# Kernel tuning notes

Measured on AMD Instinct MI355X. Metric: run time of the kernel, lower is better.

Reference implementation:

```python
import jax, jax.numpy as jnp
import numpy as np

TAU = 2.0          # LIF membrane time constant
SG_ALPHA = 4.0     # sigmoid surrogate-gradient sharpness (spikingjelly default)
TIM_ALPHA = 0.6
EPS_BN = 1e-5
NUM_HEADS = 8

@jax.custom_vjp
def spike(u):
    return (u >= 0.0).astype(u.dtype)

def _spike_fwd(u):
    return spike(u), u

def _spike_bwd(u, g):
    s = jax.nn.sigmoid(SG_ALPHA * u)
    return (g * SG_ALPHA * s * (1.0 - s),)

spike.defvjp(_spike_fwd, _spike_bwd)

def lif(x, vth):
    # Multi-step LIF over leading time axis; v_reset=0, detach_reset=True.
    def step(v, xt):
        v = v + (xt - v) / TAU
        s = spike(v - vth)
        v = v * (1.0 - jax.lax.stop_gradient(s))
        return v, s
    _, out = jax.lax.scan(step, jnp.zeros_like(x[0]), x)
    return out

def bn_c(x, p):
    # x: [T,B,C,H,W]; p: [4,C] rows = (gamma, beta, mean, var); inference BN
    g, b, m, v = p
    inv = g * jax.lax.rsqrt(v + EPS_BN)
    return inv[:, None, None] * (x - m[:, None, None]) + b[:, None, None]

def bn_last(x, p):
    # channel on last axis
    g, b, m, v = p
    return g * jax.lax.rsqrt(v + EPS_BN) * (x - m) + b

def tim(q, w, b):
    # q: [T,B,C,H,W]. Conv1d (kernel 5, pad 2) over flattened spatial dim,
    # recurrent temporal interaction, then output LIF (vth=0.5).
    T, B, C, H, W = q.shape
    x = q.reshape(T, B, C, H * W)
    dn = ('NCH', 'OIH', 'NCH')
    outs = [x[0]]
    x_tim = x[0]
    for i in range(1, T):  # T is small and fixed
        c = jax.lax.conv_general_dilated(x_tim, w, (1,), [(2, 2)], dimension_numbers=dn)
        c = c + b[None, :, None]
        s = lif(c[None], 0.3)[0]
        x_tim = s * TIM_ALPHA + x[i] * (1.0 - TIM_ALPHA)
        outs.append(x_tim)
    out = lif(jnp.stack(outs), 0.5)
    return out.reshape(T, B, C, H, W)

def dssa_forward(x, wq, wk, wv, k_bn, v_bn, dst_w, dst_bn, proj_w, proj_b, proj_bn, tim_w, tim_b):
    T, B, C, H, W = x.shape
    NH = NUM_HEADS
    hd = C // NH
    N = H * W
    identity = x

    xs = lif(x, 1.0)  # shortcut LIF
    # 1x1 convs are channel matmuls
    q = lif(jnp.einsum('tbchw,dc->tbdhw', xs, wq), 0.05)   # note: no BN on q path (as in source)
    q = tim(q, tim_w, tim_b)
    k = lif(bn_c(jnp.einsum('tbchw,dc->tbdhw', xs, wk), k_bn), 1.0)
    v = lif(bn_c(jnp.einsum('tbchw,dc->tbdhw', xs, wv), v_bn), 1.0)

    def to_heads(z):  # [T,B,C,H,W] -> [T,B,NH,N,hd]
        return z.reshape(T, B, NH, hd, N).transpose(0, 1, 2, 4, 3)
    q, k, v = to_heads(q), to_heads(k), to_heads(v)

    # dst_conv with sr_ratio=1 is a 1x1 conv on head_dim channels; shared dst_bn
    k_t = bn_last(jnp.einsum('tbhnd,ed->tbhne', k, dst_w), dst_bn)
    v_t = bn_last(jnp.einsum('tbhnd,ed->tbhne', v, dst_w), dst_bn)

    attn = jnp.einsum('tbhnd,tbhmd->tbhnm', q, k_t)
    c1 = jnp.minimum(1.0 / jnp.sqrt(q.mean() * hd + 1e-6), 10.0)  # firing-rate scale
    attn_map = lif(attn * c1, 0.5)  # spiking attention map

    out = jnp.einsum('tbhnm,tbhmd->tbhnd', attn_map, v_t)
    out = out.transpose(0, 1, 2, 4, 3).reshape(T, B, C, H, W)
    out = out + identity
    out = jnp.einsum('tbchw,dc->tbdhw', out, proj_w) + proj_b[None, None, :, None, None]
    out = lif(bn_c(out, proj_bn), 1.0)
    return out, v


def setup_inputs() -> dict:
    key = jax.random.key(0)
    ks = jax.random.split(key, 12)
    T, B, C, H, W = 4, 16, 384, 16, 16
    hd = C // NUM_HEADS

    def bn_params(k, c):
        return jnp.stack([
            jnp.ones((c,), jnp.float32),                              # gamma
            jnp.zeros((c,), jnp.float32),                             # beta
            0.1 * jax.random.normal(k, (c,), jnp.float32),            # running mean
            0.5 + jax.random.uniform(jax.random.fold_in(k, 1), (c,), jnp.float32),  # running var
        ])

    s = (2.0 / C) ** 0.5
    return {
        'x': jax.random.normal(ks[0], (T, B, C, H, W), jnp.float32),
        'wq': s * jax.random.normal(ks[1], (C, C), jnp.float32),
        'wk': s * jax.random.normal(ks[2], (C, C), jnp.float32),
        'wv': s * jax.random.normal(ks[3], (C, C), jnp.float32),
        'k_bn': bn_params(ks[4], C),
        'v_bn': bn_params(ks[5], C),
        'dst_w': (2.0 / hd) ** 0.5 * jax.random.normal(ks[6], (hd, hd), jnp.float32),
        'dst_bn': bn_params(ks[7], hd),
        'proj_w': s * jax.random.normal(ks[8], (C, C), jnp.float32),
        'proj_b': jnp.zeros((C,), jnp.float32),
        'proj_bn': bn_params(ks[9], C),
        'tim_w': (2.0 / (C * 5)) ** 0.5 * jax.random.normal(ks[10], (C, C, 5), jnp.float32),
        'tim_b': jnp.zeros((C,), jnp.float32),
    }


def reference(x, wq, wk, wv, k_bn, v_bn, dst_w, dst_bn, proj_w, proj_b, proj_bn, tim_w, tim_b):
    return dssa_forward(x, wq, wk, wv, k_bn, v_bn, dst_w, dst_bn, proj_w, proj_b, proj_bn, tim_w, tim_b)
```

## Files before the change

kernel.cpp:

```cpp
#include <hip/hip_runtime.h>
#include <math.h>

#define TT 4
#define BB 16
#define CC 384
#define NS 256
#define NHD 8
#define HDD 48
#define PLANE 98304
#define TSTR  1572864
#define TOT   6291456
#define CCSQ  147456
#define PB    99840
#define PPL   1597440

#define OFF_XS   0L
#define OFF_Q    (1L*TOT)
#define OFF_K    (2L*TOT)
#define OFF_V    (3L*TOT)
#define OFF_OUTS (4L*TOT)
#define OFF_KTS  (11L*TOT/2)
#define OFF_VT   (7L*TOT)
#define OFF_CNT  (8L*TOT)

#define NPART 6144

typedef __attribute__((ext_vector_type(8))) short short8;
typedef __attribute__((ext_vector_type(4))) float f32x4;

__device__ __forceinline__ ushort f2bf(float x) {
    union { float f; unsigned u; } c; c.f = x;
    unsigned r = c.u + 0x7FFFu + ((c.u >> 16) & 1u);
    return (ushort)(r >> 16);
}
__device__ __forceinline__ float bf2f(ushort h) {
    union { unsigned u; float f; } c; c.u = ((unsigned)h) << 16;
    return c.f;
}

__global__ __launch_bounds__(256) void k_lif_x_t(const float* __restrict__ x,
                                                 ushort* __restrict__ xs)
{
    int b = blockIdx.z, c0 = blockIdx.y*64, n0 = blockIdx.x*64;
    __shared__ ushort T[64][72];
    int tid = threadIdx.x;
    int row = tid >> 2;
    int col4 = tid & 3;

    float v[16];
    #pragma unroll
    for (int i = 0; i < 16; i++) v[i] = 0.f;

    for (int t = 0; t < TT; t++) {
        __syncthreads();
        #pragma unroll
        for (int rep = 0; rep < 4; rep++) {
            int j = col4 + rep*4;
            float4 xv = *(const float4*)&x[(long)t*TSTR + (long)b*PLANE + (long)(c0+row)*NS + n0 + j*4];
            #pragma unroll
            for (int jj = 0; jj < 4; jj++) {
                int idx = rep*4 + jj;
                float xt = ((const float*)&xv)[jj];
                float vv = v[idx];
                vv += (xt - vv)*0.5f;
                float s = (vv - 1.0f) >= 0.f ? 1.f : 0.f;
                T[j*4+jj][row] = (s != 0.f) ? (ushort)0x3F80 : (ushort)0;
                v[idx] = vv*(1.f - s);
            }
        }
        __syncthreads();
        #pragma unroll
        for (int rep = 0; rep < 2; rep++) {
            int nrow = tid >> 2;
            int cq = (tid & 3) + rep*4;
            *(uint4*)&xs[(long)t*TSTR + (long)b*PLANE + (long)(n0+nrow)*CC + c0 + cq*8]
                = *(uint4*)&T[nrow][cq*8];
        }
    }
}

__global__ __launch_bounds__(256) void k_zero_pads(unsigned* __restrict__ qspT_u32)
{
    int i = blockIdx.x*256 + threadIdx.x;
    int plane = i / 768, rem = i % 768;
    int r = rem / 192, cu = rem % 192;
    int row = (r < 2) ? r : (256 + r);
    qspT_u32[(long)plane*(PB/2) + row*192 + cu] = 0;
}

__global__ __launch_bounds__(256) void k_wsplit(
    const float* __restrict__ wq, const float* __restrict__ wk, const float* __restrict__ wv,
    ushort* __restrict__ wsp)
{
    int i = blockIdx.x*256 + threadIdx.x;
    int which = i / CCSQ, r = i % CCSQ;
    const float* W = (which==0) ? wq : (which==1 ? wk : wv);
    float v = W[r];
    ushort hi = f2bf(v);  float r1 = v - bf2f(hi);
    ushort md = f2bf(r1); float r2 = r1 - bf2f(md);
    ushort lo = f2bf(r2);
    long b = (long)which*3*CCSQ;
    wsp[b + r] = hi; wsp[b + CCSQ + r] = md; wsp[b + 2L*CCSQ + r] = lo;
}

__global__ __launch_bounds__(256) void k_wsplit_tim(const float* __restrict__ tw,
                                                    ushort* __restrict__ timw)
{
    int i = blockIdx.x*256 + threadIdx.x;
    const float* src = tw + (long)i*5;
    #pragma unroll
    for (int tap = 0; tap < 5; tap++) {
        float v = src[tap];
        ushort hi = f2bf(v);  float r1 = v - bf2f(hi);
        ushort md = f2bf(r1); float r2 = r1 - bf2f(md);
        ushort lo = f2bf(r2);
        timw[(long)(0*5 + tap)*CCSQ + i] = hi;
        timw[(long)(1*5 + tap)*CCSQ + i] = md;
        timw[(long)(2*5 + tap)*CCSQ + i] = lo;
    }
}

__global__ __launch_bounds__(512) void k_gemm_qkv_mfma(
    const ushort* __restrict__ wsp,
    const float* __restrict__ kbn, const float* __restrict__ vbn,
    const ushort* __restrict__ xs,
    float* __restrict__ qo, float* __restrict__ ko, float* __restrict__ vo)
{
    int which = blockIdx.y >> 6;
    int tb    = blockIdx.y & 63;
    const ushort* X = xs + (long)tb*PLANE;
    const ushort* Wb = wsp + (long)which*3*CCSQ;
    int d0 = blockIdx.x*64;

    __shared__ ushort Ws[3][64][40];
    __shared__ ushort Xs[256][40];

    int tid = threadIdx.x, lane = tid & 63, w = tid >> 6;
    int q4 = lane >> 4, l16 = lane & 15;
    int dstrip = w & 3, nh = w >> 2;

    f32x4 acc[8];
    #pragma unroll
    for (int nt = 0; nt < 8; nt++) acc[nt] = (f32x4){0.f,0.f,0.f,0.f};

    for (int k0 = 0; k0 < CC; k0 += 32) {
        __syncthreads();
        for (int idx = tid; idx < 1792; idx += 512) {
            if (idx < 768) {
                int pl = idx >> 8, rem = idx & 255;
                int d = rem >> 2, c8 = rem & 3;
                *(uint4*)&Ws[pl][d][c8*8] =
                    *(const uint4*)(Wb + (long)pl*CCSQ + (long)(d0+d)*CC + k0 + c8*8);
            } else {
                int j = idx - 768;
                int n = j >> 2, c8 = j & 3;
                *(uint4*)&Xs[n][c8*8] = *(const uint4*)(X + (long)n*CC + k0 + c8*8);
            }
        }
        __syncthreads();

        short8 wh = *(short8*)&Ws[0][dstrip*16 + l16][q4*8];
        short8 wm = *(short8*)&Ws[1][dstrip*16 + l16][q4*8];
        short8 wl = *(short8*)&Ws[2][dstrip*16 + l16][q4*8];
        #pragma unroll
        for (int nt = 0; nt < 8; nt++) {
            short8 xr = *(short8*)&Xs[nh*128 + nt*16 + l16][q4*8];
            acc[nt] = __builtin_amdgcn_mfma_f32_16x16x32_bf16(xr, wh, acc[nt], 0, 0, 0);
            acc[nt] = __builtin_amdgcn_mfma_f32_16x16x32_bf16(xr, wm, acc[nt], 0, 0, 0);
            acc[nt] = __builtin_amdgcn_mfma_f32_16x16x32_bf16(xr, wl, acc[nt], 0, 0, 0);
        }
    }

    float* Y = ((which==0) ? qo : (which==1 ? ko : vo)) + (long)tb*PLANE;
    int d = d0 + dstrip*16 + l16;
    float inv = 1.f, mu = 0.f, be = 0.f;
    if (which != 0) {
        const float* bn = (which==1) ? kbn : vbn;
        float g = bn[d]; be = bn[CC+d]; mu = bn[2*CC+d]; float va = bn[3*CC+d];
        inv = g / sqrtf(va + 1e-5f);
    }
    #pragma unroll
    for (int nt = 0; nt < 8; nt++) {
        #pragma unroll
        for (int r = 0; r < 4; r++) {
            int n = nh*128 + nt*16 + q4*4 + r;
            float v = acc[nt][r];
            if (which != 0) v = inv*(v - mu) + be;
            Y[(long)n*CC + d] = v;
        }
    }
}

__global__ __launch_bounds__(256) void k_lif_qkv(
    const float* __restrict__ qb, const float* __restrict__ kb, const float* __restrict__ vb,
    ushort* __restrict__ qspT, ushort* __restrict__ ksp, ushort* __restrict__ vsp,
    float* __restrict__ vout)
{
    int which = blockIdx.y;
    int i = blockIdx.x*256 + threadIdx.x;
    const float* rbuf = (which==0) ? qb : (which==1 ? kb : vb);
    float vth  = (which==0) ? 0.05f : 1.0f;
    int b = i / PLANE;
    long qofs = (long)i + b*1536 + 768;
    int c=0, n2=0, h=0, dd=0;
    if (which == 2) {
        c = i % CC; n2 = (i / CC) % NS;
        h = c / HDD; dd = c % HDD;
    }
    float v = 0.f;
    #pragma unroll
    for (int t = 0; t < TT; t++) {
        float xt = rbuf[t*TSTR + i];
        v += (xt - v)*0.5f;
        float s = (v - vth) >= 0.f ? 1.f : 0.f;
        ushort sb = (s != 0.f) ? (ushort)0x3F80 : (ushort)0;
        if (which == 0)      qspT[(long)t*PPL + qofs] = sb;
        else if (which == 1) ksp[(long)t*TSTR + i] = sb;
        else {
            vsp[(long)t*TSTR + i] = sb;
            vout[(((long)(t*BB+b)*NHD + h)*NS + n2)*HDD + dd] = s;
        }
        v *= (1.f - s);
    }
}

__global__ __launch_bounds__(512) void k_tim_conv_mfma(
    const ushort* __restrict__ timw, const float* __restrict__ bias,
    const ushort* __restrict__ qT,
    const ushort* __restrict__ sTp,
    int hass,
    ushort* __restrict__ sTo)
{
    int b = blockIdx.z, d0 = blockIdx.y*64, n0 = blockIdx.x*64;
    const ushort* qp = qT  + (long)b*PB;
    const ushort* sp = sTp + (long)b*PB;

    __shared__ ushort Xs[2][68][40];

    int tid = threadIdx.x, lane = tid & 63, w = tid >> 6;
    int q4 = lane >> 4, l16 = lane & 15;
    int dstrip = w >> 1, nh = w & 1;

    const ushort* wb = timw + (long)(d0 + dstrip*16 + l16)*CC;

    f32x4 accQ[2], accS[2];
    #pragma unroll
    for (int nt = 0; nt < 2; nt++) {
        accQ[nt] = (f32x4){0.f,0.f,0.f,0.f};
        accS[nt] = (f32x4){0.f,0.f,0.f,0.f};
    }

    for (int c0 = 0; c0 < CC; c0 += 32) {
        __syncthreads();
        int tot = hass ? 544 : 272;
        for (int idx = tid; idx < tot; idx += 512) {
            int tsel = (idx >= 272) ? 1 : 0;
            int rr = idx - tsel*272;
            int r = rr >> 2, c8 = rr & 3;
            const ushort* src = (tsel ? sp : qp) + (long)(n0 + r)*CC + c0 + c8*8;
            *(uint4*)&Xs[tsel][r][c8*8] = *(const uint4*)src;
        }
        __syncthreads();

        #pragma unroll
        for (int tap = 0; tap < 5; tap++) {
            short8 w0 = *(const short8*)(wb + (long)(0*5 + tap)*CCSQ + c0 + q4*8);
            short8 w1 = *(const short8*)(wb + (long)(1*5 + tap)*CCSQ + c0 + q4*8);
            short8 w2 = *(const short8*)(wb + (long)(2*5 + tap)*CCSQ + c0 + q4*8);
            #pragma unroll
            for (int nt = 0; nt < 2; nt++) {
                int row = nh*32 + nt*16 + l16 + tap;
                short8 aq = *(short8*)&Xs[0][row][q4*8];
                accQ[nt] = __builtin_amdgcn_mfma_f32_16x16x32_bf16(aq, w0, accQ[nt], 0, 0, 0);
                accQ[nt] = __builtin_amdgcn_mfma_f32_16x16x32_bf16(aq, w1, accQ[nt], 0, 0, 0);
                accQ[nt] = __builtin_amdgcn_mfma_f32_16x16x32_bf16(aq, w2, accQ[nt], 0, 0, 0);
                if (hass) {
                    short8 as = *(short8*)&Xs[1][row][q4*8];
                    accS[nt] = __builtin_amdgcn_mfma_f32_16x16x32_bf16(as, w0, accS[nt], 0, 0, 0);
                    accS[nt] = __builtin_amdgcn_mfma_f32_16x16x32_bf16(as, w1, accS[nt], 0, 0, 0);
                    accS[nt] = __builtin_amdgcn_mfma_f32_16x16x32_bf16(as, w2, accS[nt], 0, 0, 0);
                }
            }
        }
    }

    ushort* so = sTo + (long)b*PB;
    int d = d0 + dstrip*16 + l16;
    float bv = bias[d];
    #pragma unroll
    for (int nt = 0; nt < 2; nt++) {
        #pragma unroll
        for (int r = 0; r < 4; r++) {
            int n = n0 + nh*32 + nt*16 + q4*4 + r;
            float conv = hass ? (0.6f*accS[nt][r] + 0.4f*accQ[nt][r]) : accQ[nt][r];
            float c = conv + bv;
            float s = (c*0.5f - 0.3f) >= 0.f ? 1.f : 0.f;
            so[(long)(n + 2)*CC + d] = (s != 0.f) ? (ushort)0x3F80 : (ushort)0;
        }
    }
}

__global__ __launch_bounds__(256) void k_tim_lif(const ushort* __restrict__ qspT,
                                                 const ushort* __restrict__ splT,
                                                 ushort* __restrict__ qtim,
                                                 unsigned* __restrict__ partials)
{
    int i = blockIdx.x*256 + threadIdx.x;
    int b = i / PLANE;
    long po = (long)i + b*1536 + 768;
    float v = 0.f; unsigned c = 0;
    #pragma unroll
    for (int t = 0; t < TT; t++) {
        float val;
        if (t == 0) {
            val = bf2f(qspT[po]);
        } else {
            float sf = bf2f(splT[(long)(t-1)*PPL + po]);
            float qf = bf2f(qspT[(long)t*PPL + po]);
            val = sf*0.6f + qf*0.4f;
        }
        v += (val - v)*0.5f;
        float s = (v - 0.5f) >= 0.f ? 1.f : 0.f;
        qtim[(long)t*TSTR + i] = (s != 0.f) ? (ushort)0x3F80 : (ushort)0;
        c += (unsigned)s;
        v *= (1.f - s);
    }
    #pragma unroll
    for (int off = 32; off >= 1; off >>= 1) c += __shfl_down(c, off, 64);
    __shared__ unsigned wsum[4];
    if ((threadIdx.x & 63) == 0) wsum[threadIdx.x >> 6] = c;
    __syncthreads();
    if (threadIdx.x == 0)
        partials[blockIdx.x] = wsum[0] + wsum[1] + wsum[2] + wsum[3];
}

__global__ __launch_bounds__(256) void k_cnt_reduce(const unsigned* __restrict__ partials,
                                                    unsigned* __restrict__ cnt)
{
    unsigned c = 0;
    for (int i = threadIdx.x; i < NPART; i += 256) c += partials[i];
    #pragma unroll
    for (int off = 32; off >= 1; off >>= 1) c += __shfl_down(c, off, 64);
    __shared__ unsigned wsum[4];
    if ((threadIdx.x & 63) == 0) wsum[threadIdx.x >> 6] = c;
    __syncthreads();
    if (threadIdx.x == 0)
        cnt[0] = wsum[0] + wsum[1] + wsum[2] + wsum[3];
}

__global__ __launch_bounds__(256) void k_dst_mfma(
    const float* __restrict__ dw, const float* __restrict__ dbn,
    const ushort* __restrict__ ksp, const ushort* __restrict__ vsp,
    ushort* __restrict__ kth, ushort* __restrict__ ktm, ushort* __restrict__ ktl,
    ushort* __restrict__ vth, ushort* __restrict__ vtm, ushort* __restrict__ vtl)
{
    int isv = blockIdx.x;
    int tbh = blockIdx.y;
    int tb = tbh >> 3, h = tbh & 7;
    const ushort* src = (isv ? vsp : ksp) + (long)tb*PLANE + h*HDD;

    __shared__ ushort Ws[3][48][72];

    int tid = threadIdx.x, lane = tid & 63, w = tid >> 6;
    int q4 = lane >> 4, l16 = lane & 15;

    for (int idx = tid; idx < 1728; idx += 256) {
        int pl = idx / 576, rem = idx % 576;
        int e = rem / 12, cu = rem % 12;
        *(unsigned*)&Ws[pl][e][48 + cu*2] = 0;
    }
    for (int idx = tid; idx < 2304; idx += 256) {
        int e = idx / 48, d = idx % 48;
        float v = dw[idx];
        ushort hi = f2bf(v);  float r1 = v - bf2f(hi);
        ushort md = f2bf(r1); float r2 = r1 - bf2f(md);
        ushort lo = f2bf(r2);
        Ws[0][e][d] = hi; Ws[1][e][d] = md; Ws[2][e][d] = lo;
    }
    __syncthreads();

    f32x4 acc[3][4];
    #pragma unroll
    for (int es = 0; es < 3; es++)
        #pragma unroll
        for (int nt = 0; nt < 4; nt++) acc[es][nt] = (f32x4){0.f,0.f,0.f,0.f};

    #pragma unroll
    for (int k0 = 0; k0 < 64; k0 += 32) {
        short8 a[3][3];
        #pragma unroll
        for (int pl = 0; pl < 3; pl++)
            #pragma unroll
            for (int es = 0; es < 3; es++)
                a[pl][es] = *(short8*)&Ws[pl][es*16 + l16][k0 + q4*8];
        #pragma unroll
        for (int nt = 0; nt < 4; nt++) {
            int n = w*64 + nt*16 + l16;
            short8 xr = *(const short8*)(src + (long)n*CC + k0 + q4*8);
            #pragma unroll
            for (int es = 0; es < 3; es++) {
                acc[es][nt] = __builtin_amdgcn_mfma_f32_16x16x32_bf16(a[0][es], xr, acc[es][nt], 0, 0, 0);
                acc[es][nt] = __builtin_amdgcn_mfma_f32_16x16x32_bf16(a[1][es], xr, acc[es][nt], 0, 0, 0);
                acc[es][nt] = __builtin_amdgcn_mfma_f32_16x16x32_bf16(a[2][es], xr, acc[es][nt], 0, 0, 0);
            }
        }
    }

    #pragma unroll
    for (int es = 0; es < 3; es++) {
        #pragma unroll
        for (int r = 0; r < 4; r++) {
            int e = es*16 + q4*4 + r;
            float g = dbn[e], be = dbn[48+e], mu = dbn[96+e], va = dbn[144+e];
            float inv = g / sqrtf(va + 1e-5f);
            #pragma unroll
            for (int nt = 0; nt < 4; nt++) {
                int n = w*64 + nt*16 + l16;
                float val = inv*(acc[es][nt][r] - mu) + be;
                ushort hi = f2bf(val);  float r1 = val - bf2f(hi);
                ushort md = f2bf(r1);   float r2 = r1 - bf2f(md);
                ushort lo = f2bf(r2);
                if (isv) {
                    long gi = ((long)tbh*HDD + e)*NS + n;
                    vth[gi] = hi; vtm[gi] = md; vtl[gi] = lo;
                } else {
                    long gi = ((long)tbh*NS + n)*HDD + e;
                    kth[gi] = hi; ktm[gi] = md; ktl[gi] = lo;
                }
            }
        }
    }
}

__global__ __launch_bounds__(256) void k_attn_mfma(
    const ushort* __restrict__ qtim,
    const ushort* __restrict__ kth, const ushort* __restrict__ ktm, const ushort* __restrict__ ktl,
    const unsigned* __restrict__ cnt, unsigned char* __restrict__ amap)
{
    int bh = blockIdx.z;
    int b = bh >> 3, h = bh & 7;
    int nbase = blockIdx.y*64, mbase = blockIdx.x*64;

    __shared__ ushort Qs[64][72];
    __shared__ ushort Kh[64][72];
    __shared__ ushort Km[64][72];
    __shared__ ushort Kl[64][72];

    int tid  = threadIdx.x;
    int lane = tid & 63, w = tid >> 6;
    int q4 = lane >> 4, l16 = lane & 15;

    float mean = (float)(*cnt) / 6291456.0f;
    float c1 = fminf(1.0f / sqrtf(mean*48.0f + 1e-6f), 10.0f);

    {
        unsigned* z0 = (unsigned*)&Qs[0][0];
        unsigned* z1 = (unsigned*)&Kh[0][0];
        unsigned* z2 = (unsigned*)&Km[0][0];
        unsigned* z3 = (unsigned*)&Kl[0][0];
        for (int i2 = tid; i2 < 64*72/2; i2 += 256) {
            z0[i2] = 0; z1[i2] = 0; z2[i2] = 0; z3[i2] = 0;
        }
    }

    float vmem[4][4];
    #pragma unroll
    for (int a = 0; a < 4; a++)
        #pragma unroll
        for (int r = 0; r < 4; r++) vmem[a][r] = 0.f;

    for (int t = 0; t < TT; t++) {
        int tb = t*BB + b;
        __syncthreads();
        const ushort* qsrc = qtim + (long)tb*PLANE + (long)nbase*CC + h*HDD;
        for (int idx = tid; idx < 768; idx += 256) {
            int n = idx / 12, c4 = idx % 12;
            *(uint2*)&Qs[n][c4*4] = *(const uint2*)(qsrc + (long)n*CC + c4*4);
        }
        long kb0 = ((long)(tb*NHD + h)*NS + mbase)*HDD;
        const ushort* kbh = kth + kb0;
        const ushort* kbm = ktm + kb0;
        const ushort* kbl = ktl + kb0;
        for (int idx = tid; idx < 1536; idx += 256) {
            int e2 = idx << 1;
            int m = e2 / HDD, er = e2 % HDD;
            *(unsigned*)&Kh[m][er] = *(const unsigned*)(kbh + e2);
            *(unsigned*)&Km[m][er] = *(const unsigned*)(kbm + e2);
            *(unsigned*)&Kl[m][er] = *(const unsigned*)(kbl + e2);
        }
        __syncthreads();

        int nrow = w*16 + l16;
        f32x4 acc[4];
        #pragma unroll
        for (int mt = 0; mt < 4; mt++) acc[mt] = (f32x4){0.f, 0.f, 0.f, 0.f};

        #pragma unroll
        for (int ks = 0; ks < 2; ks++) {
            short8 a = *(short8*)&Qs[nrow][ks*32 + q4*8];
            #pragma unroll
            for (int mt = 0; mt < 4; mt++) {
                int mrow = mt*16 + l16;
                short8 b_h = *(short8*)&Kh[mrow][ks*32 + q4*8];
                short8 b_m = *(short8*)&Km[mrow][ks*32 + q4*8];
                short8 b_l = *(short8*)&Kl[mrow][ks*32 + q4*8];
                acc[mt] = __builtin_amdgcn_mfma_f32_16x16x32_bf16(a, b_h, acc[mt], 0, 0, 0);
                acc[mt] = __builtin_amdgcn_mfma_f32_16x16x32_bf16(a, b_m, acc[mt], 0, 0, 0);
                acc[mt] = __builtin_amdgcn_mfma_f32_16x16x32_bf16(a, b_l, acc[mt], 0, 0, 0);
            }
        }

        long abase0 = ((long)(tb*NHD + h)*NS)*NS;
        #pragma unroll
        for (int mt = 0; mt < 4; mt++) {
            int m = mbase + mt*16 + l16;
            #pragma unroll
            for (int r = 0; r < 4; r++) {
                int n = nbase + w*16 + q4*4 + r;
                float a = acc[mt][r]*c1;
                float v = vmem[mt][r];
                v += (a - v)*0.5f;
                float s = (v - 0.5f) >= 0.f ? 1.f : 0.f;
                amap[abase0 + (long)n*NS + m] = (unsigned char)s;
                vmem[mt][r] = v*(1.f - s);
            }
        }
    }
}

__global__ __launch_bounds__(512) void k_outmm_mfma(
    const unsigned char* __restrict__ amap,
    const ushort* __restrict__ vth, const ushort* __restrict__ vtm, const ushort* __restrict__ vtl,
    const float* __restrict__ x, float* __restrict__ oid)
{
    int tbh = blockIdx.x;
    int tb = tbh >> 3, h = tbh & 7;
    int tid = threadIdx.x, lane = tid & 63, w = tid >> 6;
    int q4 = lane >> 4, l16 = lane & 15;
    int nbase = w*32;

    long vbase = (long)tbh*HDD*NS;

    f32x4 acc[2][3];
    #pragma unroll
    for (int nt = 0; nt < 2; nt++)
        #pragma unroll
        for (int et = 0; et < 3; et++) acc[nt][et] = (f32x4){0.f,0.f,0.f,0.f};

    for (int k0 = 0; k0 < NS; k0 += 32) {
        short8 a[2];
        #pragma unroll
        for (int nt = 0; nt < 2; nt++) {
            const unsigned char* arow = amap + ((long)tbh*NS + nbase + nt*16 + l16)*NS;
            uint2 u = *(const uint2*)(arow + k0 + q4*8);
            #pragma unroll
            for (int j = 0; j < 4; j++) {
                a[nt][j]   = ((u.x >> (8*j)) & 0xFFu) ? (short)0x3F80 : (short)0;
                a[nt][j+4] = ((u.y >> (8*j)) & 0xFFu) ? (short)0x3F80 : (short)0;
            }
        }
        #pragma unroll
        for (int et = 0; et < 3; et++) {
            long vo = vbase + (long)(et*16 + l16)*NS + k0 + q4*8;
            short8 bh = *(const short8*)(vth + vo);
            short8 bm = *(const short8*)(vtm + vo);
            short8 bl = *(const short8*)(vtl + vo);
            #pragma unroll
            for (int nt = 0; nt < 2; nt++) {
                acc[nt][et] = __builtin_amdgcn_mfma_f32_16x16x32_bf16(a[nt], bh, acc[nt][et], 0, 0, 0);
                acc[nt][et] = __builtin_amdgcn_mfma_f32_16x16x32_bf16(a[nt], bm, acc[nt][et], 0, 0, 0);
                acc[nt][et] = __builtin_amdgcn_mfma_f32_16x16x32_bf16(a[nt], bl, acc[nt][et], 0, 0, 0);
            }
        }
    }
    #pragma unroll
    for (int nt = 0; nt < 2; nt++) {
        #pragma unroll
        for (int et = 0; et < 3; et++) {
            int e = et*16 + l16;
            int n = nbase + nt*16 + q4*4;
            long base = (long)tb*PLANE + (long)(h*HDD + e)*NS + n;
            float4 xi = *(const float4*)(x + base);
            float4 o4;
            o4.x = acc[nt][et][0] + xi.x;
            o4.y = acc[nt][et][1] + xi.y;
            o4.z = acc[nt][et][2] + xi.z;
            o4.w = acc[nt][et][3] + xi.w;
            *(float4*)(oid + base) = o4;
        }
    }
}

__global__ __launch_bounds__(256) void k_gemm_proj(
    const float* __restrict__ W, const float* __restrict__ bias, const float* __restrict__ bn,
    const float* __restrict__ Xfull, float* __restrict__ Yfull)
{
    int tb = blockIdx.z;
    const float* X = Xfull + (long)tb*PLANE;
    float* Y = Yfull + (long)tb*PLANE;
    int d0 = blockIdx.y*64, n0 = blockIdx.x*64;

    __shared__ float As[16][68];
    __shared__ float Bs[16][68];
    int tid = threadIdx.x;
    int ty = tid >> 4, tx = tid & 15;
    float acc[4][4] = {};

    for (int k0 = 0; k0 < CC; k0 += 16) {
        {
            int d = tid >> 2, kq = (tid & 3)*4;
            float4 a4 = *(const float4*)&W[(long)(d0+d)*CC + k0 + kq];
            As[kq+0][d]=a4.x; As[kq+1][d]=a4.y; As[kq+2][d]=a4.z; As[kq+3][d]=a4.w;
        }
        {
            int k = tid >> 4, nq = (tid & 15)*4;
            *(float4*)&Bs[k][nq] = *(const float4*)&X[(long)(k0+k)*NS + n0 + nq];
        }
        __syncthreads();
        #pragma unroll
        for (int kk = 0; kk < 16; kk++) {
            float a0=As[kk][ty*4+0], a1=As[kk][ty*4+1], a2=As[kk][ty*4+2], a3=As[kk][ty*4+3];
            float b0=Bs[kk][tx*4+0], b1=Bs[kk][tx*4+1], b2=Bs[kk][tx*4+2], b3=Bs[kk][tx*4+3];
            acc[0][0]+=a0*b0; acc[0][1]+=a0*b1; acc[0][2]+=a0*b2; acc[0][3]+=a0*b3;
            acc[1][0]+=a1*b0; acc[1][1]+=a1*b1; acc[1][2]+=a1*b2; acc[1][3]+=a1*b3;
            acc[2][0]+=a2*b0; acc[2][1]+=a2*b1; acc[2][2]+=a2*b2; acc[2][3]+=a2*b3;
            acc[3][0]+=a3*b0; acc[3][1]+=a3*b1; acc[3][2]+=a3*b2; acc[3][3]+=a3*b3;
        }
        __syncthreads();
    }
    #pragma unroll
    for (int i = 0; i < 4; i++) {
        int d = d0 + ty*4 + i;
        float g = bn[d], be = bn[CC+d], mu = bn[2*CC+d], va = bn[3*CC+d];
        float inv = g / sqrtf(va + 1e-5f);
        float bv = bias[d];
        float4 o4;
        o4.x = inv*((acc[i][0]+bv) - mu) + be;
        o4.y = inv*((acc[i][1]+bv) - mu) + be;
        o4.z = inv*((acc[i][2]+bv) - mu) + be;
        o4.w = inv*((acc[i][3]+bv) - mu) + be;
        *(float4*)&Y[(long)d*NS + n0 + tx*4] = o4;
    }
}

__global__ __launch_bounds__(256) void k_final_lif(const float* __restrict__ pre,
                                                   float* __restrict__ out)
{
    int i = blockIdx.x*256 + threadIdx.x;
    float v = 0.f;
    #pragma unroll
    for (int t = 0; t < TT; t++) {
        float xt = pre[t*TSTR + i];
        v += (xt - v)*0.5f;
        float s = (v - 1.0f) >= 0.f ? 1.f : 0.f;
        out[t*TSTR + i] = s;
        v *= (1.f - s);
    }
}

extern "C" void kernel_launch(void* const* d_in, const int* in_sizes, int n_in,
                              void* d_out, int out_size, void* d_ws, size_t ws_size,
                              hipStream_t stream) {
    const float* x   = (const float*)d_in[0];
    const float* wq  = (const float*)d_in[1];
    const float* wk  = (const float*)d_in[2];
    const float* wv  = (const float*)d_in[3];
    const float* kbn = (const float*)d_in[4];
    const float* vbn = (const float*)d_in[5];
    const float* dw  = (const float*)d_in[6];
    const float* dbn = (const float*)d_in[7];
    const float* pw  = (const float*)d_in[8];
    const float* pb  = (const float*)d_in[9];
    const float* pbn = (const float*)d_in[10];
    const float* tw  = (const float*)d_in[11];
    const float* tbi = (const float*)d_in[12];

    float* out  = (float*)d_out;
    float* vout = out + TOT;

    float* ws   = (float*)d_ws;
    ushort* xs  = (ushort*)(ws + OFF_XS);
    float* oid  = ws + OFF_XS;
    float* qb   = ws + OFF_Q;
    float* kb   = ws + OFF_K;
    float* vb   = ws + OFF_V;
    ushort* qtim = (ushort*)(ws + OFF_Q);
    ushort* vtl  = (ushort*)(ws + OFF_Q) + TOT;
    ushort* qspT = (ushort*)(ws + OFF_OUTS);
    ushort* splT = qspT + 4L*PPL;
    ushort* ksp  = qspT + 7L*PPL;
    unsigned char* amap = (unsigned char*)(ws + OFF_OUTS);
    ushort* vsp = (ushort*)d_out;
    unsigned* partials = (unsigned*)(ws + OFF_KTS);
    ushort* wsp  = (ushort*)(ws + OFF_KTS) + 32768;
    ushort* timw = wsp + 9L*CCSQ;
    ushort* kth = (ushort*)(ws + OFF_KTS);
    ushort* ktm = kth + TOT;
    ushort* ktl = kth + 2L*TOT;
    ushort* vth = (ushort*)(ws + OFF_VT);
    ushort* vtm = vth + TOT;
    unsigned* cnt = (unsigned*)(ws + OFF_CNT);

    k_lif_x_t<<<dim3(4, 6, 16), 256, 0, stream>>>(x, xs);
    k_wsplit<<<dim3(3*CCSQ/256), 256, 0, stream>>>(wq, wk, wv, wsp);
    k_wsplit_tim<<<dim3(CCSQ/256), 256, 0, stream>>>(tw, timw);
    k_zero_pads<<<dim3(336), 256, 0, stream>>>((unsigned*)qspT);
    k_gemm_qkv_mfma<<<dim3(6, 192), 512, 0, stream>>>(wsp, kbn, vbn, xs, qb, kb, vb);
    k_lif_qkv<<<dim3(TSTR/256, 3), 256, 0, stream>>>(qb, kb, vb, qspT, ksp, vsp, vout);
    for (int i = 1; i < TT; i++) {
        k_tim_conv_mfma<<<dim3(4, 6, 16), 512, 0, stream>>>(
            timw, tbi,
            qspT + (long)(i-1)*PPL,
            (i >= 2) ? (splT + (long)(i-2)*PPL) : qspT ,
            (i >= 2) ? 1 : 0,
            splT + (long)(i-1)*PPL);
    }
    k_tim_lif<<<dim3(NPART), 256, 0, stream>>>(qspT, splT, qtim, partials);
    k_cnt_reduce<<<dim3(1), 256, 0, stream>>>(partials, cnt);
    k_dst_mfma<<<dim3(2, 512), 256, 0, stream>>>(dw, dbn, ksp, vsp, kth, ktm, ktl, vth, vtm, vtl);
    k_attn_mfma<<<dim3(4, 4, 128), 256, 0, stream>>>(qtim, kth, ktm, ktl, cnt, amap);
    k_outmm_mfma<<<dim3(512), 512, 0, stream>>>(amap, vth, vtm, vtl, x, oid);
    k_gemm_proj<<<dim3(4, 6, 64), 256, 0, stream>>>(pw, pb, pbn, oid, kb);
    k_final_lif<<<dim3(TSTR/256), 256, 0, stream>>>(kb, out);
}
```

Before: 701.6 us.

## Hoist q-side TIM convolutions into one batched launch off the recurrence

```diff
diff --git a/kernel.cpp b/kernel.cpp
--- a/kernel.cpp
+++ b/kernel.cpp
@@ -224,18 +224,18 @@
     }
 }
 
-__global__ __launch_bounds__(512) void k_tim_conv_mfma(
+__global__ __launch_bounds__(512) void k_tim_convq_mfma(
     const ushort* __restrict__ timw, const float* __restrict__ bias,
-    const ushort* __restrict__ qT,
-    const ushort* __restrict__ sTp,
-    int hass,
-    ushort* __restrict__ sTo)
-{
-    int b = blockIdx.z, d0 = blockIdx.y*64, n0 = blockIdx.x*64;
-    const ushort* qp = qT  + (long)b*PB;
-    const ushort* sp = sTp + (long)b*PB;
-
-    __shared__ ushort Xs[2][68][40];
+    const ushort* __restrict__ qspT,
+    ushort* __restrict__ s1out,
+    float* __restrict__ cq)
+{
+    int z = blockIdx.z;
+    int t = z >> 4, b = z & 15;
+    int d0 = blockIdx.y*64, n0 = blockIdx.x*64;
+    const ushort* qp = qspT + (long)t*PPL + (long)b*PB;
+
+    __shared__ ushort Xs[68][40];
 
     int tid = threadIdx.x, lane = tid & 63, w = tid >> 6;
     int q4 = lane >> 4, l16 = lane & 15;
@@ -243,22 +243,15 @@
 
     const ushort* wb = timw + (long)(d0 + dstrip*16 + l16)*CC;
 
-    f32x4 accQ[2], accS[2];
-    #pragma unroll
-    for (int nt = 0; nt < 2; nt++) {
-        accQ[nt] = (f32x4){0.f,0.f,0.f,0.f};
-        accS[nt] = (f32x4){0.f,0.f,0.f,0.f};
-    }
+    f32x4 accQ[2];
+    accQ[0] = (f32x4){0.f,0.f,0.f,0.f};
+    accQ[1] = (f32x4){0.f,0.f,0.f,0.f};
 
     for (int c0 = 0; c0 < CC; c0 += 32) {
         __syncthreads();
-        int tot = hass ? 544 : 272;
-        for (int idx = tid; idx < tot; idx += 512) {
-            int tsel = (idx >= 272) ? 1 : 0;
-            int rr = idx - tsel*272;
-            int r = rr >> 2, c8 = rr & 3;
-            const ushort* src = (tsel ? sp : qp) + (long)(n0 + r)*CC + c0 + c8*8;
-            *(uint4*)&Xs[tsel][r][c8*8] = *(const uint4*)src;
+        for (int idx = tid; idx < 272; idx += 512) {
+            int r = idx >> 2, c8 = idx & 3;
+            *(uint4*)&Xs[r][c8*8] = *(const uint4*)(qp + (long)(n0 + r)*CC + c0 + c8*8);
         }
         __syncthreads();
 
@@ -270,21 +263,88 @@
             #pragma unroll
             for (int nt = 0; nt < 2; nt++) {
                 int row = nh*32 + nt*16 + l16 + tap;
-                short8 aq = *(short8*)&Xs[0][row][q4*8];
+                short8 aq = *(short8*)&Xs[row][q4*8];
                 accQ[nt] = __builtin_amdgcn_mfma_f32_16x16x32_bf16(aq, w0, accQ[nt], 0, 0, 0);
                 accQ[nt] = __builtin_amdgcn_mfma_f32_16x16x32_bf16(aq, w1, accQ[nt], 0, 0, 0);
                 accQ[nt] = __builtin_amdgcn_mfma_f32_16x16x32_bf16(aq, w2, accQ[nt], 0, 0, 0);
-                if (hass) {
-                    short8 as = *(short8*)&Xs[1][row][q4*8];
-                    accS[nt] = __builtin_amdgcn_mfma_f32_16x16x32_bf16(as, w0, accS[nt], 0, 0, 0);
-                    accS[nt] = __builtin_amdgcn_mfma_f32_16x16x32_bf16(as, w1, accS[nt], 0, 0, 0);
-                    accS[nt] = __builtin_amdgcn_mfma_f32_16x16x32_bf16(as, w2, accS[nt], 0, 0, 0);
-                }
+            }
+        }
+    }
+
+    int d = d0 + dstrip*16 + l16;
+    if (t == 0) {
+        ushort* so = s1out + (long)b*PB;
+        float bv = bias[d];
+        #pragma unroll
+        for (int nt = 0; nt < 2; nt++) {
+            #pragma unroll
+            for (int r = 0; r < 4; r++) {
+                int n = n0 + nh*32 + nt*16 + q4*4 + r;
+                float c = accQ[nt][r] + bv;
+                float s = (c*0.5f - 0.3f) >= 0.f ? 1.f : 0.f;
+                so[(long)(n + 2)*CC + d] = (s != 0.f) ? (ushort)0x3F80 : (ushort)0;
+            }
+        }
+    } else {
+        float* co = cq + (long)(t-1)*TSTR + (long)b*PLANE;
+        #pragma unroll
+        for (int nt = 0; nt < 2; nt++) {
+            #pragma unroll
+            for (int r = 0; r < 4; r++) {
+                int n = n0 + nh*32 + nt*16 + q4*4 + r;
+                co[(long)n*CC + d] = accQ[nt][r];
+            }
+        }
+    }
+}
+
+__global__ __launch_bounds__(256) void k_tim_convs_mfma(
+    const ushort* __restrict__ timw, const float* __restrict__ bias,
+    const ushort* __restrict__ sTp,
+    const float* __restrict__ cq,
+    ushort* __restrict__ sTo)
+{
+    int b = blockIdx.z, d0 = blockIdx.y*32, n0 = blockIdx.x*64;
+    const ushort* sp = sTp + (long)b*PB;
+
+    __shared__ ushort Xs[68][40];
+
+    int tid = threadIdx.x, lane = tid & 63, w = tid >> 6;
+    int q4 = lane >> 4, l16 = lane & 15;
+    int dstrip = w >> 1, nh = w & 1;
+
+    const ushort* wb = timw + (long)(d0 + dstrip*16 + l16)*CC;
+
+    f32x4 accS[2];
+    accS[0] = (f32x4){0.f,0.f,0.f,0.f};
+    accS[1] = (f32x4){0.f,0.f,0.f,0.f};
+
+    for (int c0 = 0; c0 < CC; c0 += 32) {
+        __syncthreads();
+        for (int idx = tid; idx < 272; idx += 256) {
+            int r = idx >> 2, c8 = idx & 3;
+            *(uint4*)&Xs[r][c8*8] = *(const uint4*)(sp + (long)(n0 + r)*CC + c0 + c8*8);
+        }
+        __syncthreads();
+
+        #pragma unroll
+        for (int tap = 0; tap < 5; tap++) {
+            short8 w0 = *(const short8*)(wb + (long)(0*5 + tap)*CCSQ + c0 + q4*8);
+            short8 w1 = *(const short8*)(wb + (long)(1*5 + tap)*CCSQ + c0 + q4*8);
+            short8 w2 = *(const short8*)(wb + (long)(2*5 + tap)*CCSQ + c0 + q4*8);
+            #pragma unroll
+            for (int nt = 0; nt < 2; nt++) {
+                int row = nh*32 + nt*16 + l16 + tap;
+                short8 as = *(short8*)&Xs[row][q4*8];
+                accS[nt] = __builtin_amdgcn_mfma_f32_16x16x32_bf16(as, w0, accS[nt], 0, 0, 0);
+                accS[nt] = __builtin_amdgcn_mfma_f32_16x16x32_bf16(as, w1, accS[nt], 0, 0, 0);
+                accS[nt] = __builtin_amdgcn_mfma_f32_16x16x32_bf16(as, w2, accS[nt], 0, 0, 0);
             }
         }
     }
 
     ushort* so = sTo + (long)b*PB;
+    const float* co = cq + (long)b*PLANE;
     int d = d0 + dstrip*16 + l16;
     float bv = bias[d];
     #pragma unroll
@@ -292,7 +352,7 @@
         #pragma unroll
         for (int r = 0; r < 4; r++) {
             int n = n0 + nh*32 + nt*16 + q4*4 + r;
-            float conv = hass ? (0.6f*accS[nt][r] + 0.4f*accQ[nt][r]) : accQ[nt][r];
+            float conv = 0.6f*accS[nt][r] + 0.4f*co[(long)n*CC + d];
             float c = conv + bv;
             float s = (c*0.5f - 0.3f) >= 0.f ? 1.f : 0.f;
             so[(long)(n + 2)*CC + d] = (s != 0.f) ? (ushort)0x3F80 : (ushort)0;
@@ -682,6 +742,7 @@
     ushort* xs  = (ushort*)(ws + OFF_XS);
     float* oid  = ws + OFF_XS;
     float* qb   = ws + OFF_Q;
+    float* cq   = ws + OFF_Q;
     float* kb   = ws + OFF_K;
     float* vb   = ws + OFF_V;
     ushort* qtim = (ushort*)(ws + OFF_Q);
@@ -707,12 +768,12 @@
     k_zero_pads<<<dim3(336), 256, 0, stream>>>((unsigned*)qspT);
     k_gemm_qkv_mfma<<<dim3(6, 192), 512, 0, stream>>>(wsp, kbn, vbn, xs, qb, kb, vb);
     k_lif_qkv<<<dim3(TSTR/256, 3), 256, 0, stream>>>(qb, kb, vb, qspT, ksp, vsp, vout);
-    for (int i = 1; i < TT; i++) {
-        k_tim_conv_mfma<<<dim3(4, 6, 16), 512, 0, stream>>>(
+    k_tim_convq_mfma<<<dim3(4, 6, 48), 512, 0, stream>>>(timw, tbi, qspT, splT, cq);
+    for (int i = 2; i <= 3; i++) {
+        k_tim_convs_mfma<<<dim3(4, 12, 16), 256, 0, stream>>>(
             timw, tbi,
-            qspT + (long)(i-1)*PPL,
-            (i >= 2) ? (splT + (long)(i-2)*PPL) : qspT ,
-            (i >= 2) ? 1 : 0,
+            splT + (long)(i-2)*PPL,
+            cq + (long)(i-2)*TSTR,
             splT + (long)(i-1)*PPL);
     }
     k_tim_lif<<<dim3(NPART), 256, 0, stream>>>(qspT, splT, qtim, partials);
```

After: 779.9 us. +11.2%, slower.
